# Kernel tuning notes

Measured on AMD Instinct MI355X. Metric: run time of the kernel, lower is better.

The kernel has to match this reference:

```python
import jax, jax.numpy as jnp
import numpy as np

NEG = -1e30  # finite stand-in for -inf (safe under grads)


def setup_inputs() -> dict:
    key = jax.random.key(0)
    k0, k1, k2, k3 = jax.random.split(key, 4)
    B, L, NS, NG = 32, 1024, 32768, 64
    spans = jax.random.randint(k0, (B, NS, 2), 0, L)
    span_scores = jax.random.normal(k1, (B, NS), dtype=jnp.float32)
    gold_spans = jax.random.randint(k2, (B, NG, 2), 0, L)
    gold_span_labels = jax.random.randint(k3, (B, NG), 0, 2)
    span_mask = jnp.ones((B, NS), jnp.float32)
    gold_span_mask = jnp.ones((B, NG), jnp.float32)
    token_mask = jnp.ones((B, L), jnp.float32)
    return {
        "spans": spans,
        "span_scores": span_scores,
        "gold_spans": gold_spans,
        "gold_span_labels": gold_span_labels,
        "span_mask": span_mask,
        "gold_span_mask": gold_span_mask,
        "token_mask": token_mask,
    }


def _span_table(spans, span_scores, L):
    # T[b, s, e] = sum of span_scores over list entries with (start, end) == (s, e)
    B = span_scores.shape[0]
    b = jnp.arange(B)[:, None]
    T = jnp.zeros((B, L, L), span_scores.dtype)
    return T.at[b, spans[..., 0], spans[..., 1]].add(span_scores)


def _log_denominator(T, token_mask):
    # semi-Markov CRF forward algorithm.
    # beta[i] = logsumexp over last-segment-start j of alpha[i, j]; the original
    # DP only consumes alpha rows through their row-logsumexp, so:
    # beta[i] = logsumexp({beta[s] + S(s, i-1) : s < i} U {beta[i-1] - S(i-1, i-1)})
    B, L = token_mask.shape

    def step(beta, i):
        row = jax.lax.dynamic_index_in_dim(T, i - 1, axis=2, keepdims=False)  # (B, L): S(s, i-1)
        valid = jnp.arange(L) < i
        cand = jnp.where(valid[None, :], beta[:, :L] + row, NEG)
        lse_plus = jax.nn.logsumexp(cand, axis=1)                             # (B,)
        beta_prev = jax.lax.dynamic_index_in_dim(beta, i - 1, axis=1, keepdims=False)
        diag = jax.lax.dynamic_index_in_dim(row, i - 1, axis=1, keepdims=False)  # S(i-1, i-1)
        new_val = jnp.logaddexp(lse_plus, beta_prev - diag)
        beta = jax.lax.dynamic_update_index_in_dim(beta, new_val, i, axis=1)
        return beta, None

    beta0 = jnp.full((B, L + 1), NEG, T.dtype).at[:, 0].set(0.0)
    beta, _ = jax.lax.scan(step, beta0, jnp.arange(1, L + 1))
    n = token_mask.sum(-1).astype(jnp.int32)  # valid length per batch element
    return jnp.take_along_axis(beta, n[:, None], axis=1)[:, 0]


def _log_numerator(T, gold_spans, gold_span_labels, gold_span_mask):
    B = T.shape[0]
    b = jnp.arange(B)[:, None]
    vals = T[b, gold_spans[..., 0], gold_spans[..., 1]]  # (B, NG)
    signs = 2.0 * gold_span_labels.astype(T.dtype) - 1.0
    return jnp.sum(vals * gold_span_mask * signs, axis=1)


def reference(spans, span_scores, gold_spans, gold_span_labels, span_mask, gold_span_mask, token_mask):
    # span_mask is accepted (as in the original forward signature) but unused
    # by the likelihood math in the source.
    L = token_mask.shape[1]
    T = _span_table(spans, span_scores, L)
    log_den = _log_denominator(T, token_mask)
    log_num = _log_numerator(T, gold_spans, gold_span_labels, gold_span_mask)
    return jnp.sum(log_num - log_den)
```

## Files before the change

### kernel.cpp

```cpp
#include <hip/hip_runtime.h>


#define B_   32
#define L_   1024
#define NS_  32768
#define NG_  64
#define CAP_ 128
#define NREC 128

#define DPP_ADD(v, ctrl) \
    ((v) + __int_as_float(__builtin_amdgcn_update_dpp( \
        0, __float_as_int(v), (ctrl), 0xf, 0xf, false)))

__device__ __forceinline__ float wave_sum64(float v) {
    v = DPP_ADD(v, 0x111);
    v = DPP_ADD(v, 0x112);
    v = DPP_ADD(v, 0x114);
    v = DPP_ADD(v, 0x118);
    v = DPP_ADD(v, 0x142);
    v = DPP_ADD(v, 0x143);
    return __int_as_float(__builtin_amdgcn_readlane(__float_as_int(v), 63));
}

__global__ void sbc_scatter(const int2* __restrict__ spans,
                            const float* __restrict__ scores,
                            unsigned int* __restrict__ keys,
                            float* __restrict__ vals) {
    int idx = blockIdx.x * blockDim.x + threadIdx.x;
    if (idx >= B_ * NS_) return;
    int b = idx >> 15;
    int2 se = spans[idx];
    float sc = scores[idx];
    size_t col = ((size_t)b << 10) | (unsigned)se.y;
    unsigned int* kcol = keys + col * CAP_;
    float*        vcol = vals + col * CAP_;
    unsigned int key = (unsigned int)se.x + 1u;
    int h = se.x & (CAP_ - 1);
    for (int p = 0; p < CAP_; ++p) {
        unsigned int old = atomicCAS(&kcol[h], 0u, key);
        if (old == 0u || old == key) { atomicAdd(&vcol[h], sc); break; }
        h = (h + 1) & (CAP_ - 1);
    }
}

__global__ void __launch_bounds__(256) sbc_prep(const unsigned int* __restrict__ keys,
                                                const float* __restrict__ vals,
                                                uint2* __restrict__ rec) {
    const int wv = threadIdx.x >> 6;
    const int lane = threadIdx.x & 63;
    __shared__ uint2 st[4][NREC];
    __shared__ float dnr[4][8];
    const int step = gridDim.x * 4;
    for (int col = blockIdx.x * 4 + wv; col < B_ * L_; col += step) {
        const int e = col & (L_ - 1);
        const unsigned int* kcol = keys + (size_t)col * CAP_;
        const float*        vcol = vals + (size_t)col * CAP_;
        ((uint4*)st[wv])[lane] = make_uint4(0u, 0u, 0u, 0u);
        if (lane < 8) dnr[wv][lane] = 0.f;
        int cnt = 0;
        #pragma unroll
        for (int r = 0; r < 2; ++r) {
            int slot = lane + r * 64;
            unsigned int k = kcol[slot];
            float v = vcol[slot];
            bool occ = (k != 0u);
            int s = (int)k - 1;
            int t = e - s;
            if (occ && t >= 0 && t <= 4) atomicAdd(&dnr[wv][t], v);
            bool far = occ && (t >= 5);
            unsigned long long mb = __ballot(far);
            int pos = cnt + (int)__popcll(mb & ((1ull << lane) - 1ull));
            if (far && pos < NREC - 4)
                st[wv][4 + pos] = make_uint2((unsigned)s, __float_as_uint(expm1f(v)));
            cnt += (int)__popcll(mb);
        }
        if (lane == 0) {
            float d = dnr[wv][0];
            st[wv][0] = make_uint2(__float_as_uint(__expf(d) + __expf(-d) - 1.f),
                                   __float_as_uint(expm1f(dnr[wv][1])));
            st[wv][1] = make_uint2(__float_as_uint(expm1f(dnr[wv][2])),
                                   __float_as_uint(expm1f(dnr[wv][3])));
            st[wv][2] = make_uint2(__float_as_uint(expm1f(dnr[wv][4])), 0u);
        }
        ((uint4*)(rec + (size_t)col * NREC))[lane] = ((const uint4*)st[wv])[lane];
    }
}

__global__ void __launch_bounds__(64) sbc_gold(const unsigned int* __restrict__ keys,
                                               const float* __restrict__ vals,
                                               const int2* __restrict__ gold,
                                               const int* __restrict__ labels,
                                               const float* __restrict__ gmask,
                                               float* __restrict__ num) {
    const int b = blockIdx.x;
    const int lane = threadIdx.x;
    const int gi = b * NG_ + lane;
    int2 se = gold[gi];
    const size_t col = ((size_t)b << 10) | (unsigned)se.y;
    const unsigned int* kcol = keys + col * CAP_;
    const float*        vcol = vals + col * CAP_;
    unsigned int key = (unsigned int)se.x + 1u;
    int h = se.x & (CAP_ - 1);
    float v = 0.f;
    for (int p = 0; p < CAP_; ++p) {
        unsigned int k = kcol[h];
        if (k == key) { v = vcol[h]; break; }
        if (k == 0u) break;
        h = (h + 1) & (CAP_ - 1);
    }
    float acc = v * gmask[gi] * (2.f * (float)labels[gi] - 1.f);
    #pragma unroll
    for (int o = 32; o; o >>= 1) acc += __shfl_xor(acc, o, 64);
    if (lane == 0) num[b] = acc;
}

__global__ void __launch_bounds__(64) sbc_dp(const uint2* __restrict__ rec,
                                             const float* __restrict__ tmask,
                                             float* __restrict__ den) {
    const int b = blockIdx.x;
    const int lane = threadIdx.x;
    __shared__ float xs[L_ + 1];
    const uint4* pb = (const uint4*)rec + (size_t)b * L_ * (NREC / 2);

    if (lane == 0) xs[0] = 1.f;

    float tm = 0.f;
    for (int t = lane; t < L_; t += 64) tm += tmask[b * L_ + t];
    #pragma unroll
    for (int o = 32; o; o >>= 1) tm += __shfl_xor(tm, o, 64);
    int n = (int)(tm + 0.5f);
    n = (n > L_) ? L_ : n;

    float scC[4], sc1[4], sc2[4], sc3[4], sc4[4];
    #pragma unroll
    for (int c = 0; c < 4; ++c) {
        uint4 t = pb[c * 64 + lane];
        scC[c] = __uint_as_float(__builtin_amdgcn_readlane((int)t.x, 0));
        sc1[c] = __uint_as_float(__builtin_amdgcn_readlane((int)t.y, 0));
        sc2[c] = __uint_as_float(__builtin_amdgcn_readlane((int)t.z, 0));
        sc3[c] = __uint_as_float(__builtin_amdgcn_readlane((int)t.w, 0));
        sc4[c] = __uint_as_float(__builtin_amdgcn_readlane((int)t.x, 1));
    }
    uint4 pkS[8];
    #pragma unroll
    for (int k = 0; k < 8; ++k)
        pkS[(4 + k) & 7] = pb[(4 + k) * 64 + lane];

    float gS[4] = {0.f, 0.f, 0.f, 0.f};
    float Kcur = 0.f;
    float P = 1.f, m = 0.f;
    float xm1 = 1.f, xm2 = 0.f, xm3 = 0.f, xm4 = 0.f, xm5 = 0.f;
    const bool gl = (lane >= 2);

    for (int ii = 0; ii < L_; ii += 8) {
        #pragma unroll
        for (int Kc = 0; Kc < 8; ++Kc) {
            const int e = ii + Kc;
            const float mc = scC[Kc & 3], m1 = sc1[Kc & 3], m2 = sc2[Kc & 3],
                        m3 = sc3[Kc & 3], m4 = sc4[Kc & 3];
            float Knext = wave_sum64(gS[(Kc + 1) & 3]);
            uint4 pk = pkS[(Kc + 4) & 7];
            int   s0 = gl ? (int)pk.x : 0;
            int   s1 = gl ? (int)pk.z : 0;
            float w0 = gl ? __uint_as_float(pk.y) : 0.f;
            float w1 = gl ? __uint_as_float(pk.w) : 0.f;
            float p = w0 * xs[s0] + w1 * xs[s1];
            scC[Kc & 3] = __uint_as_float(__builtin_amdgcn_readlane((int)pk.x, 0));
            sc1[Kc & 3] = __uint_as_float(__builtin_amdgcn_readlane((int)pk.y, 0));
            sc2[Kc & 3] = __uint_as_float(__builtin_amdgcn_readlane((int)pk.z, 0));
            sc3[Kc & 3] = __uint_as_float(__builtin_amdgcn_readlane((int)pk.w, 0));
            sc4[Kc & 3] = __uint_as_float(__builtin_amdgcn_readlane((int)pk.x, 1));
            gS[Kc & 3] = p;
            int cl = e + 12; cl = (cl > L_ - 1) ? (L_ - 1) : cl;
            pkS[(Kc + 4) & 7] = pb[cl * 64 + lane];
            float A = (P + Kcur) + (m1 * xm2 + m2 * xm3) + (m3 * xm4 + m4 * xm5);
            float x = fmaf(xm1, mc, A);
            if (lane == 0) xs[e + 1] = x;
            P += x;
            if (x > 0x1p64f) {
                const float s_ = 0x1p-64f;
                x *= s_; xm1 *= s_; xm2 *= s_; xm3 *= s_; xm4 *= s_;
                P *= s_; Knext *= s_;
                gS[0] *= s_; gS[1] *= s_; gS[2] *= s_; gS[3] *= s_;
                m += 44.361419555836498f;
                for (int j = lane; j <= e + 1; j += 64) xs[j] *= s_;
            }
            xm5 = xm4; xm4 = xm3; xm3 = xm2; xm2 = xm1; xm1 = x;
            Kcur = Knext;
        }
    }
    if (lane == 0) den[b] = m + logf(xs[n]);
}

__global__ void sbc_final(const float* __restrict__ num,
                          const float* __restrict__ den,
                          float* __restrict__ out) {
    int lane = threadIdx.x;
    float v = (lane < B_) ? (num[lane] - den[lane]) : 0.f;
    #pragma unroll
    for (int o = 32; o; o >>= 1) v += __shfl_xor(v, o, 64);
    if (lane == 0) out[0] = v;
}

extern "C" void kernel_launch(void* const* d_in, const int* in_sizes, int n_in,
                              void* d_out, int out_size, void* d_ws, size_t ws_size,
                              hipStream_t stream) {
    const int2*  spans       = (const int2*)d_in[0];
    const float* span_scores = (const float*)d_in[1];
    const int2*  gold        = (const int2*)d_in[2];
    const int*   glabels     = (const int*)d_in[3];
    const float* gmask       = (const float*)d_in[5];
    const float* tmask       = (const float*)d_in[6];
    float* out = (float*)d_out;
    (void)in_sizes; (void)n_in; (void)out_size; (void)ws_size;

    char* ws = (char*)d_ws;
    const size_t keysB = (size_t)B_ * L_ * CAP_ * 4;
    const size_t valsB = keysB;
    const size_t recB  = (size_t)B_ * L_ * NREC * 8;
    unsigned int* keys = (unsigned int*)(ws);
    float*        vals = (float*)(ws + keysB);
    uint2*        recp = (uint2*)(ws + keysB + valsB);
    float*        num  = (float*)(ws + keysB + valsB + recB);
    float*        den  = num + B_;

    hipMemsetAsync(keys, 0, keysB + valsB, stream);
    sbc_scatter<<<(B_ * NS_) / 256, 256, 0, stream>>>(spans, span_scores, keys, vals);
    sbc_prep<<<2048, 256, 0, stream>>>(keys, vals, recp);
    sbc_gold<<<B_, 64, 0, stream>>>(keys, vals, gold, glabels, gmask, num);
    sbc_dp<<<B_, 64, 0, stream>>>(recp, tmask, den);
    sbc_final<<<1, 64, 0, stream>>>(num, den, out);
}
```

Baseline: 363.3 us.

## Shrink DP near-diagonal window to four terms and fuse gold lookup with final reduction

The span-table prep now stores only four near-diagonal coefficients (t=0..3) in the record header, leaving two header slots instead of four. This lets the DP read its coefficients straight from the packed record instead of extracting them with readlanes, and it uses one fewer history term per step. The overflow rescale check is now driven by a wave ballot on lane 0. The gold-span lookup and final reduction are merged into one 1024-thread kernel, removing a launch, and the scatter bounds check is dropped, which relies on an exact grid size.

```diff
diff --git a/kernel.cpp b/kernel.cpp
--- a/kernel.cpp
+++ b/kernel.cpp
@@ -27,7 +27,6 @@
                             unsigned int* __restrict__ keys,
                             float* __restrict__ vals) {
     int idx = blockIdx.x * blockDim.x + threadIdx.x;
-    if (idx >= B_ * NS_) return;
     int b = idx >> 15;
     int2 se = spans[idx];
     float sc = scores[idx];
@@ -66,12 +65,12 @@
             bool occ = (k != 0u);
             int s = (int)k - 1;
             int t = e - s;
-            if (occ && t >= 0 && t <= 4) atomicAdd(&dnr[wv][t], v);
-            bool far = occ && (t >= 5);
+            if (occ && t >= 0 && t <= 3) atomicAdd(&dnr[wv][t], v);
+            bool far = occ && (t >= 4);
             unsigned long long mb = __ballot(far);
             int pos = cnt + (int)__popcll(mb & ((1ull << lane) - 1ull));
-            if (far && pos < NREC - 4)
-                st[wv][4 + pos] = make_uint2((unsigned)s, __float_as_uint(expm1f(v)));
+            if (far && pos < NREC - 2)
+                st[wv][2 + pos] = make_uint2((unsigned)s, __float_as_uint(expm1f(v)));
             cnt += (int)__popcll(mb);
         }
         if (lane == 0) {
@@ -80,38 +79,9 @@
                                    __float_as_uint(expm1f(dnr[wv][1])));
             st[wv][1] = make_uint2(__float_as_uint(expm1f(dnr[wv][2])),
                                    __float_as_uint(expm1f(dnr[wv][3])));
-            st[wv][2] = make_uint2(__float_as_uint(expm1f(dnr[wv][4])), 0u);
         }
         ((uint4*)(rec + (size_t)col * NREC))[lane] = ((const uint4*)st[wv])[lane];
     }
-}
-
-__global__ void __launch_bounds__(64) sbc_gold(const unsigned int* __restrict__ keys,
-                                               const float* __restrict__ vals,
-                                               const int2* __restrict__ gold,
-                                               const int* __restrict__ labels,
-                                               const float* __restrict__ gmask,
-                                               float* __restrict__ num) {
-    const int b = blockIdx.x;
-    const int lane = threadIdx.x;
-    const int gi = b * NG_ + lane;
-    int2 se = gold[gi];
-    const size_t col = ((size_t)b << 10) | (unsigned)se.y;
-    const unsigned int* kcol = keys + col * CAP_;
-    const float*        vcol = vals + col * CAP_;
-    unsigned int key = (unsigned int)se.x + 1u;
-    int h = se.x & (CAP_ - 1);
-    float v = 0.f;
-    for (int p = 0; p < CAP_; ++p) {
-        unsigned int k = kcol[h];
-        if (k == key) { v = vcol[h]; break; }
-        if (k == 0u) break;
-        h = (h + 1) & (CAP_ - 1);
-    }
-    float acc = v * gmask[gi] * (2.f * (float)labels[gi] - 1.f);
-    #pragma unroll
-    for (int o = 32; o; o >>= 1) acc += __shfl_xor(acc, o, 64);
-    if (lane == 0) num[b] = acc;
 }
 
 __global__ void __launch_bounds__(64) sbc_dp(const uint2* __restrict__ rec,
@@ -131,16 +101,10 @@
     int n = (int)(tm + 0.5f);
     n = (n > L_) ? L_ : n;
 
-    float scC[4], sc1[4], sc2[4], sc3[4], sc4[4];
-    #pragma unroll
-    for (int c = 0; c < 4; ++c) {
-        uint4 t = pb[c * 64 + lane];
-        scC[c] = __uint_as_float(__builtin_amdgcn_readlane((int)t.x, 0));
-        sc1[c] = __uint_as_float(__builtin_amdgcn_readlane((int)t.y, 0));
-        sc2[c] = __uint_as_float(__builtin_amdgcn_readlane((int)t.z, 0));
-        sc3[c] = __uint_as_float(__builtin_amdgcn_readlane((int)t.w, 0));
-        sc4[c] = __uint_as_float(__builtin_amdgcn_readlane((int)t.x, 1));
-    }
+    uint4 metaS[4];
+    #pragma unroll
+    for (int c = 0; c < 4; ++c)
+        metaS[c] = pb[c * 64 + lane];
     uint4 pkS[8];
     #pragma unroll
     for (int k = 0; k < 8; ++k)
@@ -149,15 +113,14 @@
     float gS[4] = {0.f, 0.f, 0.f, 0.f};
     float Kcur = 0.f;
     float P = 1.f, m = 0.f;
-    float xm1 = 1.f, xm2 = 0.f, xm3 = 0.f, xm4 = 0.f, xm5 = 0.f;
-    const bool gl = (lane >= 2);
+    float xm1 = 1.f, xm2 = 0.f, xm3 = 0.f, xm4 = 0.f;
+    const bool gl = (lane >= 1);
 
     for (int ii = 0; ii < L_; ii += 8) {
         #pragma unroll
         for (int Kc = 0; Kc < 8; ++Kc) {
             const int e = ii + Kc;
-            const float mc = scC[Kc & 3], m1 = sc1[Kc & 3], m2 = sc2[Kc & 3],
-                        m3 = sc3[Kc & 3], m4 = sc4[Kc & 3];
+            uint4 M = metaS[Kc & 3];
             float Knext = wave_sum64(gS[(Kc + 1) & 3]);
             uint4 pk = pkS[(Kc + 4) & 7];
             int   s0 = gl ? (int)pk.x : 0;
@@ -165,41 +128,74 @@
             float w0 = gl ? __uint_as_float(pk.y) : 0.f;
             float w1 = gl ? __uint_as_float(pk.w) : 0.f;
             float p = w0 * xs[s0] + w1 * xs[s1];
-            scC[Kc & 3] = __uint_as_float(__builtin_amdgcn_readlane((int)pk.x, 0));
-            sc1[Kc & 3] = __uint_as_float(__builtin_amdgcn_readlane((int)pk.y, 0));
-            sc2[Kc & 3] = __uint_as_float(__builtin_amdgcn_readlane((int)pk.z, 0));
-            sc3[Kc & 3] = __uint_as_float(__builtin_amdgcn_readlane((int)pk.w, 0));
-            sc4[Kc & 3] = __uint_as_float(__builtin_amdgcn_readlane((int)pk.x, 1));
+            metaS[Kc & 3] = pk;
             gS[Kc & 3] = p;
             int cl = e + 12; cl = (cl > L_ - 1) ? (L_ - 1) : cl;
             pkS[(Kc + 4) & 7] = pb[cl * 64 + lane];
-            float A = (P + Kcur) + (m1 * xm2 + m2 * xm3) + (m3 * xm4 + m4 * xm5);
-            float x = fmaf(xm1, mc, A);
+            float A = (P + Kcur)
+                    + (__uint_as_float(M.y) * xm2 + __uint_as_float(M.z) * xm3)
+                    + __uint_as_float(M.w) * xm4;
+            float x = fmaf(xm1, __uint_as_float(M.x), A);
             if (lane == 0) xs[e + 1] = x;
             P += x;
-            if (x > 0x1p64f) {
+            unsigned long long bm = __ballot(x > 0x1p64f);
+            if (bm & 1ull) {
                 const float s_ = 0x1p-64f;
-                x *= s_; xm1 *= s_; xm2 *= s_; xm3 *= s_; xm4 *= s_;
+                x *= s_; xm1 *= s_; xm2 *= s_; xm3 *= s_;
                 P *= s_; Knext *= s_;
                 gS[0] *= s_; gS[1] *= s_; gS[2] *= s_; gS[3] *= s_;
                 m += 44.361419555836498f;
                 for (int j = lane; j <= e + 1; j += 64) xs[j] *= s_;
             }
-            xm5 = xm4; xm4 = xm3; xm3 = xm2; xm2 = xm1; xm1 = x;
+            xm4 = xm3; xm3 = xm2; xm2 = xm1; xm1 = x;
             Kcur = Knext;
         }
     }
     if (lane == 0) den[b] = m + logf(xs[n]);
 }
 
-__global__ void sbc_final(const float* __restrict__ num,
-                          const float* __restrict__ den,
-                          float* __restrict__ out) {
-    int lane = threadIdx.x;
-    float v = (lane < B_) ? (num[lane] - den[lane]) : 0.f;
-    #pragma unroll
-    for (int o = 32; o; o >>= 1) v += __shfl_xor(v, o, 64);
-    if (lane == 0) out[0] = v;
+__global__ void __launch_bounds__(1024) sbc_goldfinal(
+        const unsigned int* __restrict__ keys,
+        const float* __restrict__ vals,
+        const int2* __restrict__ gold,
+        const int* __restrict__ labels,
+        const float* __restrict__ gmask,
+        const float* __restrict__ den,
+        float* __restrict__ out) {
+    const int wv = threadIdx.x >> 6;
+    const int lane = threadIdx.x & 63;
+    __shared__ float part[16];
+    float acc2 = 0.f;
+    #pragma unroll
+    for (int r = 0; r < 2; ++r) {
+        const int b = wv * 2 + r;
+        const int gi = b * NG_ + lane;
+        int2 se = gold[gi];
+        const size_t col = ((size_t)b << 10) | (unsigned)se.y;
+        const unsigned int* kcol = keys + col * CAP_;
+        const float*        vcol = vals + col * CAP_;
+        unsigned int key = (unsigned int)se.x + 1u;
+        int h = se.x & (CAP_ - 1);
+        float v = 0.f;
+        for (int p = 0; p < CAP_; ++p) {
+            unsigned int k = kcol[h];
+            if (k == key) { v = vcol[h]; break; }
+            if (k == 0u) break;
+            h = (h + 1) & (CAP_ - 1);
+        }
+        float acc = v * gmask[gi] * (2.f * (float)labels[gi] - 1.f);
+        #pragma unroll
+        for (int o = 32; o; o >>= 1) acc += __shfl_xor(acc, o, 64);
+        if (lane == 0) acc2 += acc - den[b];
+    }
+    if (lane == 0) part[wv] = acc2;
+    __syncthreads();
+    if (threadIdx.x < 64) {
+        float v = (lane < 16) ? part[lane] : 0.f;
+        #pragma unroll
+        for (int o = 8; o; o >>= 1) v += __shfl_xor(v, o, 64);
+        if (lane == 0) out[0] = v;
+    }
 }
 
 extern "C" void kernel_launch(void* const* d_in, const int* in_sizes, int n_in,
@@ -221,13 +217,11 @@
     unsigned int* keys = (unsigned int*)(ws);
     float*        vals = (float*)(ws + keysB);
     uint2*        recp = (uint2*)(ws + keysB + valsB);
-    float*        num  = (float*)(ws + keysB + valsB + recB);
-    float*        den  = num + B_;
+    float*        den  = (float*)(ws + keysB + valsB + recB);
 
     hipMemsetAsync(keys, 0, keysB + valsB, stream);
     sbc_scatter<<<(B_ * NS_) / 256, 256, 0, stream>>>(spans, span_scores, keys, vals);
     sbc_prep<<<2048, 256, 0, stream>>>(keys, vals, recp);
-    sbc_gold<<<B_, 64, 0, stream>>>(keys, vals, gold, glabels, gmask, num);
     sbc_dp<<<B_, 64, 0, stream>>>(recp, tmask, den);
-    sbc_final<<<1, 64, 0, stream>>>(num, den, out);
-}
+    sbc_goldfinal<<<1, 1024, 0, stream>>>(keys, vals, gold, glabels, gmask, den, out);
+}
```

Measured after the change: 378.3 us. 4.1% more time.
